# Performance work log

Measured on AMD Instinct MI355X. Metric: run time of the kernel, lower is better.

The kernel has to match this reference:

```python
import jax, jax.numpy as jnp
import numpy as np

B, H, W = 64, 128, 128
PS, G = 8, 16            # patch size, token grid (128//8)
E = 256                  # embed_dim (hidden_dim)
NS, IT, TEMP = 8, 3, 1.0 # num_slots, slot_iters, slot_temperature
V = 10                   # vocab_size
FD = 320                 # full_dim = latent_dim(256) + pose_dim(64)
HEADS, HD = 4, E // 4    # RoPE attn heads / head_dim
N = G * G


def _ln(x, g, b, eps=1e-5):
    m = x.mean(-1, keepdims=True)
    v = ((x - m) ** 2).mean(-1, keepdims=True)
    return (x - m) * jax.lax.rsqrt(v + eps) * g + b


def _conv(x, w, stride):
    return jax.lax.conv_general_dilated(
        x, w, (stride, stride), 'VALID',
        dimension_numbers=('NCHW', 'OIHW', 'NCHW'))


def _rope_tables(g, hd):
    half = hd // 2
    inv = 1.0 / (10000.0 ** (jnp.arange(0, half, 2, dtype=jnp.float32) / half))
    pos = jnp.arange(g, dtype=jnp.float32)
    p = jnp.outer(pos, inv)                                  # [g, half//2]
    e = jnp.concatenate([jnp.sin(p), jnp.cos(p)], axis=-1)   # [g, half]
    ex = jnp.broadcast_to(e[None, :, :], (g, g, half))
    ey = jnp.broadcast_to(e[:, None, :], (g, g, half))
    emb = jnp.concatenate([ey, ex], axis=-1).reshape(g * g, hd)
    return jnp.cos(emb)[None, :, None, :], jnp.sin(emb)[None, :, None, :]


def _apply_rope(x, cos, sin):
    x1, x2 = x[..., 0::2], x[..., 1::2]
    rot = jnp.concatenate([-x2, x1], axis=-1)
    return x * cos + rot * sin


def _gru(x, h, wih, whh, bih, bhh):
    gi = x @ wih.T + bih
    gh = h @ whh.T + bhh
    i_r, i_z, i_n = jnp.split(gi, 3, axis=-1)
    h_r, h_z, h_n = jnp.split(gh, 3, axis=-1)
    r = jax.nn.sigmoid(i_r + h_r)
    z = jax.nn.sigmoid(i_z + h_z)
    n = jnp.tanh(i_n + r * h_n)
    return (1.0 - z) * n + z * h


def setup_inputs() -> dict:
    key = jax.random.key(0)
    ks = iter(jax.random.split(key, 40))

    def nrm(shape, s=0.02):
        return (jax.random.normal(next(ks), shape, jnp.float32) * s)

    state = jax.random.randint(next(ks), (B, 1, H, W), 0, V).astype(jnp.float32)
    return {
        'state': state,
        'conv_w': nrm((E, 12, PS, PS)), 'conv_b': jnp.zeros((E,), jnp.float32),
        'mlp_ln_g': jnp.ones((E,), jnp.float32), 'mlp_ln_b': jnp.zeros((E,), jnp.float32),
        'mlp_w1': nrm((2 * E, E)), 'mlp_b1': jnp.zeros((2 * E,), jnp.float32),
        'mlp_w2': nrm((E, 2 * E)), 'mlp_b2': jnp.zeros((E,), jnp.float32),
        'qkv_w': nrm((3 * E, E)), 'qkv_b': jnp.zeros((3 * E,), jnp.float32),
        'proj_w': nrm((E, E)), 'proj_b': jnp.zeros((E,), jnp.float32),
        'ni_g': jnp.ones((E,), jnp.float32), 'ni_b': jnp.zeros((E,), jnp.float32),
        'ns_g': jnp.ones((FD,), jnp.float32), 'ns_b': jnp.zeros((FD,), jnp.float32),
        'nm_g': jnp.ones((FD,), jnp.float32), 'nm_b': jnp.zeros((FD,), jnp.float32),
        'q_w': nrm((FD, FD)), 'k_w': nrm((FD, E)), 'v_w': nrm((FD, E)),
        'gru_wih': nrm((3 * FD, FD)), 'gru_whh': nrm((3 * FD, FD)),
        'gru_bih': jnp.zeros((3 * FD,), jnp.float32), 'gru_bhh': jnp.zeros((3 * FD,), jnp.float32),
        'smlp_w1': nrm((2 * FD, FD)), 'smlp_b1': jnp.zeros((2 * FD,), jnp.float32),
        'smlp_w2': nrm((FD, 2 * FD)), 'smlp_b2': jnp.zeros((FD,), jnp.float32),
    }


def reference(state, conv_w, conv_b, mlp_ln_g, mlp_ln_b, mlp_w1, mlp_b1,
              mlp_w2, mlp_b2, qkv_w, qkv_b, proj_w, proj_b, ni_g, ni_b,
              ns_g, ns_b, nm_g, nm_b, q_w, k_w, v_w,
              gru_wih, gru_whh, gru_bih, gru_bhh,
              smlp_w1, smlp_b1, smlp_w2, smlp_b2):
    # Sobel edge features on replicate-padded image
    sob_x = jnp.array([[-1., 0., 1.], [-2., 0., 2.], [-1., 0., 1.]], jnp.float32).reshape(1, 1, 3, 3)
    sob_y = jnp.array([[-1., -2., -1.], [0., 0., 0.], [1., 2., 1.]], jnp.float32).reshape(1, 1, 3, 3)
    pad = jnp.pad(state, ((0, 0), (0, 0), (1, 1), (1, 1)), mode='edge')
    sx = _conv(pad, sob_x, 1)
    sy = _conv(pad, sob_y, 1)
    ids = jax.lax.stop_gradient(state)[:, 0].astype(jnp.int32)
    onehot = jax.nn.one_hot(ids, V, dtype=jnp.float32).transpose(0, 3, 1, 2)
    comp = jnp.concatenate([onehot, sx, sy], axis=1)            # [B,12,H,W]

    # Patch embed -> tokens [B,N,E]
    x = _conv(comp, conv_w, PS) + conv_b[None, :, None, None]   # [B,E,G,G]
    x = x.reshape(B, E, N).transpose(0, 2, 1)

    # patch_mlp (LN -> Linear -> GELU -> Linear), no residual
    h = _ln(x, mlp_ln_g, mlp_ln_b)
    h = jax.nn.gelu(h @ mlp_w1.T + mlp_b1, approximate=False)
    x = h @ mlp_w2.T + mlp_b2

    # RoPE self-attention, residual
    cos, sin = _rope_tables(G, HD)
    qkv = (x @ qkv_w.T + qkv_b).reshape(B, N, 3, HEADS, HD)
    q, k, v = qkv[:, :, 0], qkv[:, :, 1], qkv[:, :, 2]          # [B,N,Hh,HD]
    q = _apply_rope(q, cos, sin).transpose(0, 2, 1, 3)          # [B,Hh,N,HD]
    k = _apply_rope(k, cos, sin).transpose(0, 2, 1, 3)
    v = v.transpose(0, 2, 1, 3)
    attn = jax.nn.softmax(jnp.einsum('bhnd,bhmd->bhnm', q, k) * HD ** -0.5, axis=-1)
    ao = jnp.einsum('bhnm,bhmd->bhnd', attn, v).transpose(0, 2, 1, 3).reshape(B, N, E)
    x = x + (ao @ proj_w.T + proj_b)
    x = _ln(x, ni_g, ni_b)

    k_in = x @ k_w.T                                            # [B,N,FD]
    v_in = x @ v_w.T

    # No codebook injected -> zero slot priors
    slots = jnp.zeros((B, NS, FD), jnp.float32)
    sattn = None
    for _ in range(IT):
        slots_prev = slots
        q_s = _ln(slots, ns_g, ns_b) @ q_w.T                    # [B,NS,FD]
        logits = jnp.einsum('bnf,bsf->bns', k_in, q_s) * FD ** -0.5
        sattn = jax.nn.softmax(logits / TEMP, axis=-1)          # over slots
        an = sattn + 1e-8
        an = an / an.sum(axis=1, keepdims=True)                 # normalize over keys
        updates = jnp.einsum('bns,bnf->bsf', an, v_in)          # [B,NS,FD]
        slots = _gru(updates.reshape(-1, FD), slots_prev.reshape(-1, FD),
                     gru_wih, gru_whh, gru_bih, gru_bhh).reshape(B, NS, FD)
        m = _ln(slots, nm_g, nm_b)
        m = jax.nn.gelu(m @ smlp_w1.T + smlp_b1, approximate=False)
        slots = slots + (m @ smlp_w2.T + smlp_b2)

    masks = jax.lax.stop_gradient(sattn).transpose(0, 2, 1).reshape(B, NS, G, G)
    return slots, masks
```

## Files before the change

### kernel.cpp

```cpp
#include <hip/hip_runtime.h>
#include <math.h>

#define BB   64
#define HH   128
#define WW   128
#define GG   16
#define NN   256
#define EE   256
#define FD   320
#define NSL  8
#define NHEAD 4
#define HD   64
#define KIM  768

using short8 = __attribute__((ext_vector_type(8))) short;
using f32x4  = __attribute__((ext_vector_type(4))) float;

__device__ __forceinline__ float sigm(float x) { return 1.0f / (1.0f + expf(-x)); }
__device__ __forceinline__ float gelu_exact(float x) {
    return 0.5f * x * (1.0f + erff(x * 0.70710678118654752f));
}
__device__ __forceinline__ unsigned short f2b(float x) {
    unsigned u = __float_as_uint(x);
    u += 0x7fffu + ((u >> 16) & 1u);
    return (unsigned short)(u >> 16);
}
__device__ __forceinline__ float b2f(unsigned short u) {
    return __uint_as_float(((unsigned)u) << 16);
}
__device__ __forceinline__ void gload_lds16(const void* g, void* lds) {
    __builtin_amdgcn_global_load_lds(
        (const __attribute__((address_space(1))) unsigned int*)g,
        (__attribute__((address_space(3))) unsigned int*)lds, 16, 0, 0);
}
__device__ __forceinline__ void store_el(float* p, float v) { *p = v; }
__device__ __forceinline__ void store_el(unsigned short* p, float v) { *p = f2b(v); }

__global__ __launch_bounds__(256) void cvt_weights(
    const float* __restrict__ w0, const float* __restrict__ w1,
    const float* __restrict__ w2, const float* __restrict__ w3,
    const float* __restrict__ w4, const float* __restrict__ w5,
    const float* __restrict__ w6, const float* __restrict__ w7,
    const float* __restrict__ w8, const float* __restrict__ w9,
    const float* __restrict__ w10, const float* __restrict__ w11,
    unsigned short* __restrict__ dst) {
    int i = blockIdx.x * 256 + threadIdx.x;
    float v;
    if      (i <  196608) v = w0[i];
    else if (i <  327680) v = w1[i - 196608];
    else if (i <  458752) v = w2[i - 327680];
    else if (i <  655360) v = w3[i - 458752];
    else if (i <  720896) v = w4[i - 655360];
    else if (i <  802816) v = w5[i - 720896];
    else if (i <  884736) v = w6[i - 802816];
    else if (i <  987136) v = w7[i - 884736];
    else if (i < 1294336) v = w8[i - 987136];
    else if (i < 1601536) v = w9[i - 1294336];
    else if (i < 1806336) v = w10[i - 1601536];
    else                  v = w11[i - 1806336];
    dst[i] = f2b(v);
}

__global__ __launch_bounds__(256) void cvt_bf16(const float* __restrict__ in,
                                                unsigned short* __restrict__ out, int n) {
    int i = blockIdx.x * 256 + threadIdx.x;
    if (i < n) out[i] = f2b(in[i]);
}

__global__ __launch_bounds__(256) void rope_tab(float* __restrict__ cs,
                                                float* __restrict__ sn) {
    int i = blockIdx.x * 256 + threadIdx.x;
    int d = i & 63, n = i >> 6;
    int pos = (d < 32) ? (n >> 4) : (n & 15);
    int j = d & 31;
    float freq = powf(10000.0f, -(float)(j & 15) / 16.0f);
    float p = (float)pos * freq;
    float ang = (j < 16) ? sinf(p) : cosf(p);
    cs[i] = cosf(ang);
    sn[i] = sinf(ang);
}

__global__ __launch_bounds__(256) void sobel_im2col(const float* __restrict__ state,
                                                    unsigned short* __restrict__ X0) {
    int idx = blockIdx.x * 256 + threadIdx.x;
    if (idx >= BB * HH * WW) return;
    int w = idx % WW;
    int h = (idx / WW) % HH;
    int b = idx / (HH * WW);
    const float* st = state + (long)b * HH * WW;
    auto at = [&](int y, int x) {
        y = min(max(y, 0), HH - 1);
        x = min(max(x, 0), WW - 1);
        return st[y * WW + x];
    };
    float v00 = at(h-1, w-1), v01 = at(h-1, w), v02 = at(h-1, w+1);
    float v10 = at(h,   w-1),                  v12 = at(h,   w+1);
    float v20 = at(h+1, w-1), v21 = at(h+1, w), v22 = at(h+1, w+1);
    float sx = (v02 - v00) + 2.0f * (v12 - v10) + (v22 - v20);
    float sy = (v20 - v00) + 2.0f * (v21 - v01) + (v22 - v02);
    int id = (int)st[h * WW + w];
    int gy = h >> 3, i = h & 7, gx = w >> 3, j = w & 7;
    long row = (long)b * NN + gy * GG + gx;
    unsigned short* xr = X0 + row * KIM + i * 8 + j;
#pragma unroll
    for (int c = 0; c < 10; c++) xr[c * 64] = (id == c) ? 0x3F80u : 0u;
    xr[10 * 64] = f2b(sx);
    xr[11 * 64] = f2b(sy);
}

template <int BM, int BN, int ACT>
__global__ __launch_bounds__(256) void gemm_bf16(
    const unsigned short* __restrict__ A, const unsigned short* __restrict__ W,
    const float* __restrict__ bias, const float* __restrict__ res,
    float* __restrict__ C, unsigned short* __restrict__ Cb,
    int K, long sA, long sW, long sC1, long sC2, int cdiv, int ldc, float scale)
{
    constexpr int WN = BN / 64;
    __shared__ __align__(16) unsigned short As[BM * 32];
    __shared__ __align__(16) unsigned short Bs[BN * 32];
    const int tid = threadIdx.x;
    const int w = tid >> 6, l = tid & 63;
    const int wm = w / WN, wn = w % WN;
    const int bz = blockIdx.z;
    const unsigned short* Ab = A + (long)bz * sA + (long)(blockIdx.y * BM) * K;
    const unsigned short* Wb = W + (long)bz * sW + (long)(blockIdx.x * BN) * K;
    const long offC = (long)(bz / cdiv) * sC1 + (long)(bz % cdiv) * sC2;

    const int rA  = l >> 2;
    const int swz = ((l & 3) ^ ((l >> 3) & 3)) * 8;

    f32x4 acc[4][4] = {};

    for (int k0 = 0; k0 < K; k0 += 32) {
#pragma unroll
        for (int c = 0; c < BM / 64; c++) {
            const int chunk = w * (BM / 64) + c;
            gload_lds16(Ab + (long)(chunk * 16 + rA) * K + k0 + swz, (char*)As + chunk * 1024);
        }
#pragma unroll
        for (int c = 0; c < BN / 64; c++) {
            const int chunk = w * (BN / 64) + c;
            gload_lds16(Wb + (long)(chunk * 16 + rA) * K + k0 + swz, (char*)Bs + chunk * 1024);
        }
        __syncthreads();
        short8 af[4], bfr[4];
#pragma unroll
        for (int m = 0; m < 4; m++) {
            const int row = wm * 64 + m * 16 + (l & 15);
            const int byte = row * 64 + (((l >> 4) ^ ((row >> 1) & 3)) << 4);
            af[m] = *(const short8*)((const char*)As + byte);
        }
#pragma unroll
        for (int n = 0; n < 4; n++) {
            const int row = wn * 64 + n * 16 + (l & 15);
            const int byte = row * 64 + (((l >> 4) ^ ((row >> 1) & 3)) << 4);
            bfr[n] = *(const short8*)((const char*)Bs + byte);
        }
#pragma unroll
        for (int m = 0; m < 4; m++)
#pragma unroll
            for (int n = 0; n < 4; n++)
                acc[m][n] = __builtin_amdgcn_mfma_f32_16x16x32_bf16(af[m], bfr[n], acc[m][n], 0, 0, 0);
        __syncthreads();
    }

    const int crow0 = blockIdx.y * BM + wm * 64;
    const int ccol0 = blockIdx.x * BN + wn * 64;
#pragma unroll
    for (int m = 0; m < 4; m++) {
#pragma unroll
        for (int n = 0; n < 4; n++) {
            const int row = crow0 + m * 16 + ((l >> 4) << 2);
            const int col = ccol0 + n * 16 + (l & 15);
#pragma unroll
            for (int r = 0; r < 4; r++) {
                float v = acc[m][n][r] * scale;
                if (bias) v += bias[col];
                if (ACT == 1) v = gelu_exact(v);
                const long idx = offC + (long)(row + r) * ldc + col;
                if (res) v += res[idx];
                if (C)  C[idx] = v;
                if (Cb) Cb[idx] = f2b(v);
            }
        }
    }
}

template <int ACT>
__global__ __launch_bounds__(256) void gemm_bf16_s(
    const unsigned short* __restrict__ A, const unsigned short* __restrict__ W,
    const float* __restrict__ bias0, const float* __restrict__ bias1,
    const float* __restrict__ res,
    float* __restrict__ C, unsigned short* __restrict__ Cb,
    int K, int N, long sA, long sW, long sC, float scale)
{
    __shared__ __align__(16) unsigned short As[64 * 32];
    __shared__ __align__(16) unsigned short Bs[64 * 32];
    const int tid = threadIdx.x;
    const int w = tid >> 6, l = tid & 63;
    const int gw = l >> 4, l15 = l & 15;
    const int bz = blockIdx.z;
    const unsigned short* Ab = A + (long)bz * sA + (long)(blockIdx.y * 64) * K;
    const unsigned short* Wb = W + (long)bz * sW + (long)(blockIdx.x * 64) * K;
    const float* bias = (bz == 0) ? bias0 : bias1;
    const long offC = (long)bz * sC;

    const int rA  = l >> 2;
    const int swz = ((l & 3) ^ ((l >> 3) & 3)) * 8;

    f32x4 acc[4] = {};

    for (int k0 = 0; k0 < K; k0 += 32) {
        gload_lds16(Ab + (long)(w * 16 + rA) * K + k0 + swz, (char*)As + w * 1024);
        gload_lds16(Wb + (long)(w * 16 + rA) * K + k0 + swz, (char*)Bs + w * 1024);
        __syncthreads();
        short8 af[4];
#pragma unroll
        for (int m = 0; m < 4; m++) {
            const int row = m * 16 + l15;
            af[m] = *(const short8*)((const char*)As + row * 64 + ((gw ^ ((row >> 1) & 3)) << 4));
        }
        const int brow = w * 16 + l15;
        const short8 bf = *(const short8*)((const char*)Bs + brow * 64 + ((gw ^ ((brow >> 1) & 3)) << 4));
#pragma unroll
        for (int m = 0; m < 4; m++)
            acc[m] = __builtin_amdgcn_mfma_f32_16x16x32_bf16(af[m], bf, acc[m], 0, 0, 0);
        __syncthreads();
    }

    const int col = blockIdx.x * 64 + w * 16 + l15;
    const int row0 = blockIdx.y * 64;
#pragma unroll
    for (int m = 0; m < 4; m++) {
        const int row = row0 + m * 16 + (gw << 2);
#pragma unroll
        for (int r = 0; r < 4; r++) {
            float v = acc[m][r] * scale;
            if (bias) v += bias[col];
            if (ACT == 1) v = gelu_exact(v);
            const long idx = offC + (long)(row + r) * N + col;
            if (res) v += res[idx];
            if (C)  C[idx] = v;
            if (Cb) Cb[idx] = f2b(v);
        }
    }
}

template <typename OT>
__global__ __launch_bounds__(256) void ln_rows(const float* __restrict__ X,
                                               OT* __restrict__ Y,
                                               const float* __restrict__ g,
                                               const float* __restrict__ b,
                                               int rows, int D) {
    int gtid = blockIdx.x * 256 + threadIdx.x;
    int row = gtid >> 6;
    int lane = gtid & 63;
    if (row >= rows) return;
    const float* x = X + (long)row * D;
    const int nv = D >> 6;
    float v[5];
    float s = 0.0f;
#pragma unroll 5
    for (int i = 0; i < nv; i++) { v[i] = x[lane + (i << 6)]; s += v[i]; }
#pragma unroll
    for (int o = 32; o; o >>= 1) s += __shfl_down(s, o);
    s = __shfl(s, 0);
    float mean = s / (float)D;
    float s2 = 0.0f;
#pragma unroll 5
    for (int i = 0; i < nv; i++) { float d = v[i] - mean; s2 += d * d; }
#pragma unroll
    for (int o = 32; o; o >>= 1) s2 += __shfl_down(s2, o);
    s2 = __shfl(s2, 0);
    float inv = rsqrtf(s2 / (float)D + 1e-5f);
    OT* y = Y + (long)row * D;
#pragma unroll 5
    for (int i = 0; i < nv; i++) {
        int d = lane + (i << 6);
        store_el(&y[d], (v[i] - mean) * inv * g[d] + b[d]);
    }
}

__global__ __launch_bounds__(256) void gru_ln(const float* __restrict__ GI,
                                              const float* __restrict__ GH,
                                              float* __restrict__ slots,
                                              const float* __restrict__ g,
                                              const float* __restrict__ b,
                                              unsigned short* __restrict__ SLnb) {
    int gtid = blockIdx.x * 256 + threadIdx.x;
    int row = gtid >> 6;
    int lane = gtid & 63;
    const float* gi = GI + (long)row * 960;
    const float* gh = GH + (long)row * 960;
    float* sl = slots + (long)row * FD;
    float h[5];
    float s = 0.0f;
#pragma unroll
    for (int i = 0; i < 5; i++) {
        const int f = lane + (i << 6);
        const float rr = sigm(gi[f] + gh[f]);
        const float z  = sigm(gi[320 + f] + gh[320 + f]);
        const float nn = tanhf(gi[640 + f] + rr * gh[640 + f]);
        const float hn = (1.0f - z) * nn + z * sl[f];
        h[i] = hn;
        s += hn;
        sl[f] = hn;
    }
#pragma unroll
    for (int o = 32; o; o >>= 1) s += __shfl_down(s, o);
    s = __shfl(s, 0);
    const float mean = s * (1.0f / FD);
    float s2 = 0.0f;
#pragma unroll
    for (int i = 0; i < 5; i++) { const float d = h[i] - mean; s2 += d * d; }
#pragma unroll
    for (int o = 32; o; o >>= 1) s2 += __shfl_down(s2, o);
    s2 = __shfl(s2, 0);
    const float inv = rsqrtf(s2 * (1.0f / FD) + 1e-5f);
    unsigned short* y = SLnb + (long)row * FD;
#pragma unroll
    for (int i = 0; i < 5; i++) {
        const int f = lane + (i << 6);
        y[f] = f2b((h[i] - mean) * inv * g[f] + b[f]);
    }
}

__global__ __launch_bounds__(256) void rope_qk(const unsigned short* __restrict__ QKVb,
                                               const float* __restrict__ cs,
                                               const float* __restrict__ sn,
                                               unsigned short* __restrict__ Qr,
                                               unsigned short* __restrict__ Kr) {
    const int rid = blockIdx.x * 256 + threadIdx.x;
    const int n = rid & 255;
    const int h = (rid >> 8) & 3;
    const int b = rid >> 10;
    const unsigned short* src = QKVb + ((long)(b * 256 + n)) * 768 + h * 64;
    float cv[64], sv[64];
#pragma unroll
    for (int i = 0; i < 16; i++) {
        *(float4*)&cv[i * 4] = *(const float4*)(cs + n * 64 + i * 4);
        *(float4*)&sv[i * 4] = *(const float4*)(sn + n * 64 + i * 4);
    }
#pragma unroll
    for (int qk = 0; qk < 2; qk++) {
        const unsigned short* s0 = src + qk * 256;
        unsigned short* dst = (qk == 0 ? Qr : Kr) + (long)rid * 64;
        float x[64];
#pragma unroll
        for (int i = 0; i < 8; i++) {
            short8 v = *(const short8*)(s0 + i * 8);
#pragma unroll
            for (int j = 0; j < 8; j++) x[i * 8 + j] = b2f((unsigned short)v[j]);
        }
        unsigned short o[64];
#pragma unroll
        for (int d = 0; d < 64; d++) {
            const float rot = (d < 32) ? -x[2 * d + 1] : x[2 * (d - 32)];
            o[d] = f2b(x[d] * cv[d] + rot * sv[d]);
        }
#pragma unroll
        for (int i = 0; i < 8; i++)
            *(short8*)(dst + i * 8) = *(short8*)&o[i * 8];
    }
}

__global__ __launch_bounds__(256, 1) void fused_attn(
    const unsigned short* __restrict__ Qr,
    const unsigned short* __restrict__ Kr,
    const unsigned short* __restrict__ QKVb,
    unsigned short* __restrict__ AOb)
{
    __shared__ __align__(16) char SL[49152];
    const int h = blockIdx.x, b = blockIdx.y;
    const int tid = threadIdx.x;
    const int w = tid >> 6, l = tid & 63;
    const int gw = l >> 4, l15 = l & 15;
    const long bh = (long)b * 4 + h;
    const unsigned short* Qb = Qr + bh * NN * 64;
    const unsigned short* Kb = Kr + bh * NN * 64;
// ... 63 lines not shown
        }
        f32x4 acco[4][2] = {};
#pragma unroll
        for (int c = 0; c < 4; c++) {
#pragma unroll
            for (int nfi = 0; nfi < 4; nfi++) {
                const int nf = c * 4 + nfi;
                const int kt = nf >> 1;
                const int gr = (nf & 1) * 2 + (gw >> 1);
                const int lr = l15 + 16 * gr;
                const int j0 = (gw & 1) * 4;
#pragma unroll
                for (int mf = 0; mf < 2; mf++) {
                    uint2 pk;
                    pk.x = (unsigned)f2b(accs[nf][mf][0] * rs[mf]) |
                           ((unsigned)f2b(accs[nf][mf][1] * rs[mf]) << 16);
                    pk.y = (unsigned)f2b(accs[nf][mf][2] * rs[mf]) |
                           ((unsigned)f2b(accs[nf][mf][3] * rs[mf]) << 16);
                    *(uint2*)(Pw + ((kt & 1) * 2 + mf) * 1024 + lr * 16 + j0 * 2) = pk;
                }
            }
#pragma unroll
            for (int kti = 0; kti < 2; kti++) {
                const int kt = c * 2 + kti;
                short8 vf[4];
#pragma unroll
                for (int df = 0; df < 4; df++) {
                    const int d = df * 16 + l15;
                    vf[df] = *(const short8*)(SL + d * 512 + (((kt * 4 + gw) ^ (d & 15)) << 4));
                }
#pragma unroll
                for (int mf = 0; mf < 2; mf++) {
                    const short8 pf = *(const short8*)(Pw + (kti * 2 + mf) * 1024 + l * 16);
#pragma unroll
                    for (int df = 0; df < 4; df++)
                        acco[df][mf] = __builtin_amdgcn_mfma_f32_16x16x32_bf16(vf[df], pf, acco[df][mf], 0, 0, 0);
                }
            }
        }
#pragma unroll
        for (int df = 0; df < 4; df++)
#pragma unroll
            for (int mf = 0; mf < 2; mf++) {
                const int m = mbase + mf * 16 + l15;
                const int d = df * 16 + gw * 4;
                unsigned short o[4];
#pragma unroll
                for (int r = 0; r < 4; r++) o[r] = f2b(acco[df][mf][r]);
                *(uint2*)(AOb + ((long)(b * NN + m) * 256 + h * 64 + d)) = *(uint2*)o;
            }
    }
}

__global__ __launch_bounds__(256) void slot_logits(const float* __restrict__ Kin,
                                                   const float* __restrict__ Qs,
                                                   float* __restrict__ sattn,
                                                   float* __restrict__ sums) {
    const int b = blockIdx.x;
    const int chunk = blockIdx.y;
    __shared__ float qs[NSL][FD];
    __shared__ float colsum[NSL];
    const int tid = threadIdx.x;
    for (int i = tid; i < NSL * FD; i += 256) qs[i / FD][i % FD] = Qs[(long)b * NSL * FD + i];
    if (tid < NSL) colsum[tid] = 0.0f;
    __syncthreads();
    const int wv = tid >> 6, lane = tid & 63;
    float wsum[NSL] = {};
#pragma unroll
    for (int rr = 0; rr < 4; rr++) {
        const int r = chunk * 16 + wv * 4 + rr;
        const float* kr = Kin + ((long)b * NN + r) * FD;
        float acc[NSL] = {};
#pragma unroll
        for (int i = 0; i < 5; i++) {
            const int t = lane + (i << 6);
            const float kv = kr[t];
#pragma unroll
            for (int s = 0; s < NSL; s++) acc[s] = fmaf(kv, qs[s][t], acc[s]);
        }
#pragma unroll
        for (int s = 0; s < NSL; s++)
#pragma unroll
            for (int o = 32; o; o >>= 1) acc[s] += __shfl_down(acc[s], o);
        if (lane == 0) {
            const float scale = 0.055901699437494740f;
            float mx = -1e30f;
#pragma unroll
            for (int s = 0; s < NSL; s++) { acc[s] *= scale; mx = fmaxf(mx, acc[s]); }
            float e[NSL], sum = 0.0f;
#pragma unroll
            for (int s = 0; s < NSL; s++) { e[s] = expf(acc[s] - mx); sum += e[s]; }
            const float rsum = 1.0f / sum;
            float* outp = sattn + ((long)b * NN + r) * NSL;
#pragma unroll
            for (int s = 0; s < NSL; s++) {
                const float pp = e[s] * rsum;
                outp[s] = pp;
                wsum[s] += pp;
            }
        }
    }
    if (lane == 0) {
#pragma unroll
        for (int s = 0; s < NSL; s++) atomicAdd(&colsum[s], wsum[s]);
    }
    __syncthreads();
    if (tid < NSL) atomicAdd(&sums[b * NSL + tid], colsum[tid]);
}

__global__ __launch_bounds__(256) void slot_updates(const float* __restrict__ sattn,
                                                    const float* __restrict__ sums,
                                                    const float* __restrict__ Vin,
                                                    float* __restrict__ Upd) {
    const int b = blockIdx.x;
    const int chunk = blockIdx.y;
    const int t = threadIdx.x;
    __shared__ float an[64][NSL];
    __shared__ float inv_s[NSL];
    if (t < NSL) inv_s[t] = 1.0f / (sums[b * NSL + t] + (float)NN * 1e-8f);
    __syncthreads();
    for (int i = t; i < 64 * NSL; i += 256) {
        const int s = i & 7;
        const int n = i >> 3;
        an[n][s] = (sattn[((long)b * NN + chunk * 64 + n) * NSL + s] + 1e-8f) * inv_s[s];
    }
    __syncthreads();
    float acc[NSL][2] = {};
    const float* vb = Vin + ((long)b * NN + chunk * 64) * FD;
    for (int n = 0; n < 64; n++) {
        const float v1 = vb[(long)n * FD + t];
        const float v2 = (t < 64) ? vb[(long)n * FD + 256 + t] : 0.0f;
#pragma unroll
        for (int s = 0; s < NSL; s++) {
            const float a = an[n][s];
            acc[s][0] = fmaf(a, v1, acc[s][0]);
            acc[s][1] = fmaf(a, v2, acc[s][1]);
        }
    }
    float* ub = Upd + (long)b * NSL * FD;
#pragma unroll
    for (int s = 0; s < NSL; s++) {
        atomicAdd(&ub[s * FD + t], acc[s][0]);
        if (t < 64) atomicAdd(&ub[s * FD + 256 + t], acc[s][1]);
    }
}

__global__ __launch_bounds__(256) void write_out(const float* __restrict__ slots,
                                                 const float* __restrict__ sattn,
                                                 float* __restrict__ out) {
    int idx = blockIdx.x * 256 + threadIdx.x;
    const int SLOT_SZ = BB * NSL * FD;
    const int MASK_SZ = BB * NSL * NN;
    if (idx < SLOT_SZ) {
        out[idx] = slots[idx];
    } else if (idx < SLOT_SZ + MASK_SZ) {
        int i = idx - SLOT_SZ;
        int b = i >> 11;
        int s = (i >> 8) & 7;
        int n = i & 255;
        out[idx] = sattn[((long)b * NN + n) * NSL + s];
    }
}

extern "C" void kernel_launch(void* const* d_in, const int* in_sizes, int n_in,
                              void* d_out, int out_size, void* d_ws, size_t ws_size,
                              hipStream_t stream) {
    const float* state    = (const float*)d_in[0];
    const float* conv_w   = (const float*)d_in[1];
    const float* conv_b   = (const float*)d_in[2];
    const float* mlp_ln_g = (const float*)d_in[3];
    const float* mlp_ln_b = (const float*)d_in[4];
    const float* mlp_w1   = (const float*)d_in[5];
    const float* mlp_b1   = (const float*)d_in[6];
    const float* mlp_w2   = (const float*)d_in[7];
    const float* mlp_b2   = (const float*)d_in[8];
    const float* qkv_w    = (const float*)d_in[9];
    const float* qkv_b    = (const float*)d_in[10];
    const float* proj_w   = (const float*)d_in[11];
    const float* proj_b   = (const float*)d_in[12];
    const float* ni_g     = (const float*)d_in[13];
    const float* ni_b     = (const float*)d_in[14];
    const float* ns_g     = (const float*)d_in[15];
    const float* ns_b     = (const float*)d_in[16];
    const float* nm_g     = (const float*)d_in[17];
    const float* nm_b     = (const float*)d_in[18];
    const float* q_w      = (const float*)d_in[19];
    const float* k_w      = (const float*)d_in[20];
    const float* v_w      = (const float*)d_in[21];
    const float* gru_wih  = (const float*)d_in[22];
    const float* gru_whh  = (const float*)d_in[23];
    const float* gru_bih  = (const float*)d_in[24];
    const float* gru_bhh  = (const float*)d_in[25];
    const float* smlp_w1  = (const float*)d_in[26];
    const float* smlp_b1  = (const float*)d_in[27];
    const float* smlp_w2  = (const float*)d_in[28];
    const float* smlp_b2  = (const float*)d_in[29];

    float* ws = (float*)d_ws;
    const int M = BB * NN;
    typedef unsigned short u16;

    u16*   X0b  = (u16*)(ws + 0L);
    u16*   Qr   = (u16*)(ws + 0L);
    u16*   Kr   = (u16*)(ws + 2097152L);
    float* X1   = ws + 6291456L;
    u16*   XLNb = (u16*)(ws + 10485760L);
    u16*   Hbufb= (u16*)(ws + 12582912L);
    u16*   QKVb = (u16*)(ws + 6291456L);
    u16*   X2b  = (u16*)(ws + 23068672L);
    float* X2   = ws + 31457280L;
    u16*   Xnb  = (u16*)(ws + 31457280L);
    float* X3   = ws + 35651584L;
    float* Slots= ws + 35651584L;
    float* Qs   = ws + 35979264L;
    float* Satt = ws + 36143104L;
    float* Sums = ws + 36274176L;
    float* Upd  = ws + 36274688L;
    float* GI   = ws + 36438528L;
    float* GH   = ws + 36930048L;
    u16*   SLnb = (u16*)(ws + 37421568L);
    u16*   Updb = (u16*)(ws + 37503488L);
    u16*   Slotsb=(u16*)(ws + 37585408L);
    u16*   Mhb  = (u16*)(ws + 37667328L);
    float* Kin  = ws + 39845888L;
    float* Vin  = ws + 45088768L;
    u16*   AOb    = (u16*)(ws + 50331648L);
    u16*   wb     = (u16*)(ws + 52428800L);
    u16*   conv_wb= wb + 0;
    u16*   mlp_w1b= wb + 196608;
    u16*   mlp_w2b= wb + 327680;
    u16*   qkv_wb = wb + 458752;
    u16*   proj_wb= wb + 655360;
    u16*   k_wb   = wb + 720896;
    u16*   v_wb   = wb + 802816;
    u16*   q_wb   = wb + 884736;
    u16*   wihb   = wb + 987136;
    u16*   whhb   = wb + 1294336;
    u16*   smlp1b = wb + 1601536;
    u16*   smlp2b = wb + 1806336;
    float* CS     = ws + 53434368L;
    float* SN     = ws + 53450752L;

    float* out = (float*)d_out;

    auto gemmA = [&](const u16* A, const u16* Wt, const float* bias, const float* res,
                     float* C, u16* Cb, int Mm, int Nn, int Kk, int batch,
                     long sA, long sW, long sC1, long sC2, int cdiv, int ldc,
                     float scale, int act) {
        dim3 grid(Nn / 128, Mm / 128, batch);
        if (act) gemm_bf16<128, 128, 1><<<grid, 256, 0, stream>>>(A, Wt, bias, res, C, Cb, Kk, sA, sW, sC1, sC2, cdiv, ldc, scale);
        else     gemm_bf16<128, 128, 0><<<grid, 256, 0, stream>>>(A, Wt, bias, res, C, Cb, Kk, sA, sW, sC1, sC2, cdiv, ldc, scale);
    };
    auto gemmB = [&](const u16* A, const u16* Wt, float* C, int Mm, int Nn, int Kk) {
        dim3 grid(Nn / 64, Mm / 256, 1);
        gemm_bf16<256, 64, 0><<<grid, 256, 0, stream>>>(A, Wt, nullptr, nullptr, C, nullptr, Kk, 0, 0, 0, 0, 1, Nn, 1.0f);
    };
    auto gemmS = [&](const u16* A, const u16* Wt, const float* b0, const float* b1,
                     const float* res, float* C, u16* Cb, int Mm, int Nn, int Kk,
                     int batch, long sA, long sW, long sC, int act) {
        dim3 grid(Nn / 64, Mm / 64, batch);
        if (act) gemm_bf16_s<1><<<grid, 256, 0, stream>>>(A, Wt, b0, b1, res, C, Cb, Kk, Nn, sA, sW, sC, 1.0f);
        else     gemm_bf16_s<0><<<grid, 256, 0, stream>>>(A, Wt, b0, b1, res, C, Cb, Kk, Nn, sA, sW, sC, 1.0f);
    };

    cvt_weights<<<dim3(2011136 / 256), 256, 0, stream>>>(conv_w, mlp_w1, mlp_w2, qkv_w,
                                                         proj_w, k_w, v_w, q_w,
                                                         gru_wih, gru_whh, smlp_w1, smlp_w2, wb);
    rope_tab<<<dim3(16384 / 256), 256, 0, stream>>>(CS, SN);

    sobel_im2col<<<dim3((BB * HH * WW) / 256), 256, 0, stream>>>(state, X0b);
    gemmA(X0b, conv_wb, conv_b, nullptr, X1, nullptr, M, EE, KIM, 1, 0, 0, 0, 0, 1, EE, 1.0f, 0);
    ln_rows<u16><<<dim3(M * 64 / 256), 256, 0, stream>>>(X1, XLNb, mlp_ln_g, mlp_ln_b, M, EE);
    gemmA(XLNb, mlp_w1b, mlp_b1, nullptr, nullptr, Hbufb, M, 2 * EE, EE, 1, 0, 0, 0, 0, 1, 2 * EE, 1.0f, 1);
    gemmA(Hbufb, mlp_w2b, mlp_b2, nullptr, X2, X2b, M, EE, 2 * EE, 1, 0, 0, 0, 0, 1, EE, 1.0f, 0);
    gemmA(X2b, qkv_wb, qkv_b, nullptr, nullptr, QKVb, M, 3 * EE, EE, 1, 0, 0, 0, 0, 1, 3 * EE, 1.0f, 0);
    rope_qk<<<dim3(65536 / 256), 256, 0, stream>>>(QKVb, CS, SN, Qr, Kr);
    fused_attn<<<dim3(NHEAD, BB), 256, 0, stream>>>(Qr, Kr, QKVb, AOb);
    gemmA(AOb, proj_wb, proj_b, X2, X3, nullptr, M, EE, EE, 1, 0, 0, 0, 0, 1, EE, 1.0f, 0);
    ln_rows<u16><<<dim3(M * 64 / 256), 256, 0, stream>>>(X3, Xnb, ni_g, ni_b, M, EE);
    gemmB(Xnb, k_wb, Kin, M, FD, EE);
    gemmB(Xnb, v_wb, Vin, M, FD, EE);
    hipMemsetAsync(Slots, 0, (size_t)BB * NSL * FD * sizeof(float), stream);
    hipMemsetAsync(Slotsb, 0, (size_t)BB * NSL * FD * sizeof(u16), stream);
    for (int it = 0; it < 3; it++) {
        ln_rows<u16><<<dim3(512 * 64 / 256), 256, 0, stream>>>(Slots, SLnb, ns_g, ns_b, 512, FD);
        gemmS(SLnb, q_wb, nullptr, nullptr, nullptr, Qs, nullptr, 512, FD, FD, 1, 0, 0, 0, 0);
        hipMemsetAsync(Sums, 0, (size_t)BB * NSL * sizeof(float), stream);
        slot_logits<<<dim3(BB, 16), 256, 0, stream>>>(Kin, Qs, Satt, Sums);
        hipMemsetAsync(Upd, 0, (size_t)BB * NSL * FD * sizeof(float), stream);
        slot_updates<<<dim3(BB, 4), 256, 0, stream>>>(Satt, Sums, Vin, Upd);
        cvt_bf16<<<dim3(163840 / 256), 256, 0, stream>>>(Upd, Updb, 163840);
        gemmS(Updb, wihb, gru_bih, gru_bhh, nullptr, GI, nullptr, 512, 960, FD,
              2, 163840, 307200, 491520, 0);
        gru_ln<<<dim3(512 * 64 / 256), 256, 0, stream>>>(GI, GH, Slots, nm_g, nm_b, SLnb);
        gemmS(SLnb, smlp1b, smlp_b1, nullptr, nullptr, nullptr, Mhb, 512, 2 * FD, FD, 1, 0, 0, 0, 1);
        gemmS(Mhb, smlp2b, smlp_b2, nullptr, Slots, Slots, Slotsb, 512, FD, 2 * FD, 1, 0, 0, 0, 0);
    }
    write_out<<<dim3((BB * NSL * FD + BB * NSL * NN + 255) / 256), 256, 0, stream>>>(Slots, Satt, out);
}
```

Before: 644.1 us.

## Fuse slot-attention iterations into one per-batch persistent kernel with MFMA

Replaces the per-iteration chain of small launches (LN, q GEMM, logits, updates, convert, GRU GEMMs, GRU/LN, MLP GEMMs, output copy) with a single kernel, one block per batch element. The block keeps slots in LDS across all three iterations and does every small GEMM with bf16 MFMA. K and V projections are now written as bf16, with V transposed, so the fused kernel can stream them directly. This removes many launches, memsets and global round-trips. The cost is only 64 blocks of work, each reading weights straight from global memory, so per-block latency and low occupancy may dominate.

```diff
diff --git a/kernel.cpp b/kernel.cpp
--- a/kernel.cpp
+++ b/kernel.cpp
@@ -12,6 +12,10 @@
 #define NHEAD 4
 #define HD   64
 #define KIM  768
+
+#define K320P 328
+#define K256P 264
+#define K640P 648
 
 using short8 = __attribute__((ext_vector_type(8))) short;
 using f32x4  = __attribute__((ext_vector_type(4))) float;
@@ -61,12 +65,6 @@
     dst[i] = f2b(v);
 }
 
-__global__ __launch_bounds__(256) void cvt_bf16(const float* __restrict__ in,
-                                                unsigned short* __restrict__ out, int n) {
-    int i = blockIdx.x * 256 + threadIdx.x;
-    if (i < n) out[i] = f2b(in[i]);
-}
-
 __global__ __launch_bounds__(256) void rope_tab(float* __restrict__ cs,
                                                 float* __restrict__ sn) {
     int i = blockIdx.x * 256 + threadIdx.x;
@@ -113,7 +111,8 @@
     const unsigned short* __restrict__ A, const unsigned short* __restrict__ W,
     const float* __restrict__ bias, const float* __restrict__ res,
     float* __restrict__ C, unsigned short* __restrict__ Cb,
-    int K, long sA, long sW, long sC1, long sC2, int cdiv, int ldc, float scale)
+    int K, long sA, long sW, long sC1, long sC2, int cdiv, int ldc, float scale,
+    int tr)
 {
     constexpr int WN = BN / 64;
     __shared__ __align__(16) unsigned short As[BM * 32];
@@ -180,68 +179,12 @@
                 const long idx = offC + (long)(row + r) * ldc + col;
                 if (res) v += res[idx];
                 if (C)  C[idx] = v;
-                if (Cb) Cb[idx] = f2b(v);
-            }
-        }
-    }
-}
-
-template <int ACT>
-__global__ __launch_bounds__(256) void gemm_bf16_s(
-    const unsigned short* __restrict__ A, const unsigned short* __restrict__ W,
-    const float* __restrict__ bias0, const float* __restrict__ bias1,
-    const float* __restrict__ res,
-    float* __restrict__ C, unsigned short* __restrict__ Cb,
-    int K, int N, long sA, long sW, long sC, float scale)
-{
-    __shared__ __align__(16) unsigned short As[64 * 32];
-    __shared__ __align__(16) unsigned short Bs[64 * 32];
-    const int tid = threadIdx.x;
-    const int w = tid >> 6, l = tid & 63;
-    const int gw = l >> 4, l15 = l & 15;
-    const int bz = blockIdx.z;
-    const unsigned short* Ab = A + (long)bz * sA + (long)(blockIdx.y * 64) * K;
-    const unsigned short* Wb = W + (long)bz * sW + (long)(blockIdx.x * 64) * K;
-    const float* bias = (bz == 0) ? bias0 : bias1;
-    const long offC = (long)bz * sC;
-
-    const int rA  = l >> 2;
-    const int swz = ((l & 3) ^ ((l >> 3) & 3)) * 8;
-
-    f32x4 acc[4] = {};
-
-    for (int k0 = 0; k0 < K; k0 += 32) {
-        gload_lds16(Ab + (long)(w * 16 + rA) * K + k0 + swz, (char*)As + w * 1024);
-        gload_lds16(Wb + (long)(w * 16 + rA) * K + k0 + swz, (char*)Bs + w * 1024);
-        __syncthreads();
-        short8 af[4];
-#pragma unroll
-        for (int m = 0; m < 4; m++) {
-            const int row = m * 16 + l15;
-            af[m] = *(const short8*)((const char*)As + row * 64 + ((gw ^ ((row >> 1) & 3)) << 4));
-        }
-        const int brow = w * 16 + l15;
-        const short8 bf = *(const short8*)((const char*)Bs + brow * 64 + ((gw ^ ((brow >> 1) & 3)) << 4));
-#pragma unroll
-        for (int m = 0; m < 4; m++)
-            acc[m] = __builtin_amdgcn_mfma_f32_16x16x32_bf16(af[m], bf, acc[m], 0, 0, 0);
-        __syncthreads();
-    }
-
-    const int col = blockIdx.x * 64 + w * 16 + l15;
-    const int row0 = blockIdx.y * 64;
-#pragma unroll
-    for (int m = 0; m < 4; m++) {
-        const int row = row0 + m * 16 + (gw << 2);
-#pragma unroll
-        for (int r = 0; r < 4; r++) {
-            float v = acc[m][r] * scale;
-            if (bias) v += bias[col];
-            if (ACT == 1) v = gelu_exact(v);
-            const long idx = offC + (long)(row + r) * N + col;
-            if (res) v += res[idx];
-            if (C)  C[idx] = v;
-            if (Cb) Cb[idx] = f2b(v);
+                if (Cb) {
+                    long cidx = tr ? (((long)((row + r) >> 8) * ldc + col) * 256 + ((row + r) & 255))
+                                   : idx;
+                    Cb[cidx] = f2b(v);
+                }
+            }
         }
     }
 }
@@ -281,50 +224,6 @@
     }
 }
 
-__global__ __launch_bounds__(256) void gru_ln(const float* __restrict__ GI,
-                                              const float* __restrict__ GH,
-                                              float* __restrict__ slots,
-                                              const float* __restrict__ g,
-                                              const float* __restrict__ b,
-                                              unsigned short* __restrict__ SLnb) {
-    int gtid = blockIdx.x * 256 + threadIdx.x;
-    int row = gtid >> 6;
-    int lane = gtid & 63;
-    const float* gi = GI + (long)row * 960;
-    const float* gh = GH + (long)row * 960;
-    float* sl = slots + (long)row * FD;
-    float h[5];
-    float s = 0.0f;
-#pragma unroll
-    for (int i = 0; i < 5; i++) {
-        const int f = lane + (i << 6);
-        const float rr = sigm(gi[f] + gh[f]);
-        const float z  = sigm(gi[320 + f] + gh[320 + f]);
-        const float nn = tanhf(gi[640 + f] + rr * gh[640 + f]);
-        const float hn = (1.0f - z) * nn + z * sl[f];
-        h[i] = hn;
-        s += hn;
-        sl[f] = hn;
-    }
-#pragma unroll
-    for (int o = 32; o; o >>= 1) s += __shfl_down(s, o);
-    s = __shfl(s, 0);
-    const float mean = s * (1.0f / FD);
-    float s2 = 0.0f;
-#pragma unroll
-    for (int i = 0; i < 5; i++) { const float d = h[i] - mean; s2 += d * d; }
-#pragma unroll
-    for (int o = 32; o; o >>= 1) s2 += __shfl_down(s2, o);
-    s2 = __shfl(s2, 0);
-    const float inv = rsqrtf(s2 * (1.0f / FD) + 1e-5f);
-    unsigned short* y = SLnb + (long)row * FD;
-#pragma unroll
-    for (int i = 0; i < 5; i++) {
-        const int f = lane + (i << 6);
-        y[f] = f2b((h[i] - mean) * inv * g[f] + b[f]);
-    }
-}
-
 __global__ __launch_bounds__(256) void rope_qk(const unsigned short* __restrict__ QKVb,
                                                const float* __restrict__ cs,
                                                const float* __restrict__ sn,
@@ -494,114 +393,279 @@
     }
 }
 
-__global__ __launch_bounds__(256) void slot_logits(const float* __restrict__ Kin,
-                                                   const float* __restrict__ Qs,
-                                                   float* __restrict__ sattn,
-                                                   float* __restrict__ sums) {
+__global__ __launch_bounds__(256, 1) void fused_slots(
+    const unsigned short* __restrict__ Kinb,
+    const unsigned short* __restrict__ Vtb,
+    const unsigned short* __restrict__ q_wb,
+    const unsigned short* __restrict__ wihb,
+    const unsigned short* __restrict__ whhb,
+    const unsigned short* __restrict__ s1b,
+    const unsigned short* __restrict__ s2b,
+    const float* __restrict__ ns_g, const float* __restrict__ ns_b,
+    const float* __restrict__ nm_g, const float* __restrict__ nm_b,
+    const float* __restrict__ bih, const float* __restrict__ bhh,
+    const float* __restrict__ sb1, const float* __restrict__ sb2,
+    float* __restrict__ out)
+{
+    __shared__ float slots[8][320];
+    __shared__ __align__(16) unsigned short slotsb[16][K320P];
+    __shared__ __align__(16) unsigned short sln[16][K320P];
+    __shared__ __align__(16) char D[27136];
+    __shared__ float colsum[8];
+    __shared__ float wred[4][8];
+
+    unsigned short* q_s  = (unsigned short*)D;
+    unsigned short* updm = (unsigned short*)D;
+    float*          P    = (float*)(D + 10496);
+    unsigned short* anT  = (unsigned short*)(D + 18688);
+    unsigned short* Mh   = (unsigned short*)D;
+
     const int b = blockIdx.x;
-    const int chunk = blockIdx.y;
-    __shared__ float qs[NSL][FD];
-    __shared__ float colsum[NSL];
     const int tid = threadIdx.x;
-    for (int i = tid; i < NSL * FD; i += 256) qs[i / FD][i % FD] = Qs[(long)b * NSL * FD + i];
-    if (tid < NSL) colsum[tid] = 0.0f;
+    const int w = tid >> 6, l = tid & 63;
+    const int gw = l >> 4, l15 = l & 15;
+
+    for (int i = tid; i < 8 * 320; i += 256) ((float*)slots)[i] = 0.0f;
+    for (int i = tid; i < 8 * K320P; i += 256) {
+        ((unsigned short*)slotsb)[8 * K320P + i] = 0;
+        ((unsigned short*)sln)[8 * K320P + i] = 0;
+    }
+    for (int i = tid; i < 8 * K256P; i += 256) anT[8 * K256P + i] = 0;
     __syncthreads();
-    const int wv = tid >> 6, lane = tid & 63;
-    float wsum[NSL] = {};
-#pragma unroll
-    for (int rr = 0; rr < 4; rr++) {
-        const int r = chunk * 16 + wv * 4 + rr;
-        const float* kr = Kin + ((long)b * NN + r) * FD;
-        float acc[NSL] = {};
-#pragma unroll
-        for (int i = 0; i < 5; i++) {
-            const int t = lane + (i << 6);
-            const float kv = kr[t];
-#pragma unroll
-            for (int s = 0; s < NSL; s++) acc[s] = fmaf(kv, qs[s][t], acc[s]);
-        }
-#pragma unroll
-        for (int s = 0; s < NSL; s++)
-#pragma unroll
-            for (int o = 32; o; o >>= 1) acc[s] += __shfl_down(acc[s], o);
-        if (lane == 0) {
-            const float scale = 0.055901699437494740f;
-            float mx = -1e30f;
-#pragma unroll
-            for (int s = 0; s < NSL; s++) { acc[s] *= scale; mx = fmaxf(mx, acc[s]); }
-            float e[NSL], sum = 0.0f;
-#pragma unroll
-            for (int s = 0; s < NSL; s++) { e[s] = expf(acc[s] - mx); sum += e[s]; }
-            const float rsum = 1.0f / sum;
-            float* outp = sattn + ((long)b * NN + r) * NSL;
-#pragma unroll
-            for (int s = 0; s < NSL; s++) {
-                const float pp = e[s] * rsum;
-                outp[s] = pp;
-                wsum[s] += pp;
-            }
-        }
-    }
-    if (lane == 0) {
-#pragma unroll
-        for (int s = 0; s < NSL; s++) atomicAdd(&colsum[s], wsum[s]);
-    }
-    __syncthreads();
-    if (tid < NSL) atomicAdd(&sums[b * NSL + tid], colsum[tid]);
-}
-
-__global__ __launch_bounds__(256) void slot_updates(const float* __restrict__ sattn,
-                                                    const float* __restrict__ sums,
-                                                    const float* __restrict__ Vin,
-                                                    float* __restrict__ Upd) {
-    const int b = blockIdx.x;
-    const int chunk = blockIdx.y;
-    const int t = threadIdx.x;
-    __shared__ float an[64][NSL];
-    __shared__ float inv_s[NSL];
-    if (t < NSL) inv_s[t] = 1.0f / (sums[b * NSL + t] + (float)NN * 1e-8f);
-    __syncthreads();
-    for (int i = t; i < 64 * NSL; i += 256) {
-        const int s = i & 7;
-        const int n = i >> 3;
-        an[n][s] = (sattn[((long)b * NN + chunk * 64 + n) * NSL + s] + 1e-8f) * inv_s[s];
-    }
-    __syncthreads();
-    float acc[NSL][2] = {};
-    const float* vb = Vin + ((long)b * NN + chunk * 64) * FD;
-    for (int n = 0; n < 64; n++) {
-        const float v1 = vb[(long)n * FD + t];
-        const float v2 = (t < 64) ? vb[(long)n * FD + 256 + t] : 0.0f;
-#pragma unroll
-        for (int s = 0; s < NSL; s++) {
-            const float a = an[n][s];
-            acc[s][0] = fmaf(a, v1, acc[s][0]);
-            acc[s][1] = fmaf(a, v2, acc[s][1]);
-        }
-    }
-    float* ub = Upd + (long)b * NSL * FD;
-#pragma unroll
-    for (int s = 0; s < NSL; s++) {
-        atomicAdd(&ub[s * FD + t], acc[s][0]);
-        if (t < 64) atomicAdd(&ub[s * FD + 256 + t], acc[s][1]);
-    }
-}
-
-__global__ __launch_bounds__(256) void write_out(const float* __restrict__ slots,
-                                                 const float* __restrict__ sattn,
-                                                 float* __restrict__ out) {
-    int idx = blockIdx.x * 256 + threadIdx.x;
-    const int SLOT_SZ = BB * NSL * FD;
-    const int MASK_SZ = BB * NSL * NN;
-    if (idx < SLOT_SZ) {
-        out[idx] = slots[idx];
-    } else if (idx < SLOT_SZ + MASK_SZ) {
-        int i = idx - SLOT_SZ;
-        int b = i >> 11;
-        int s = (i >> 8) & 7;
-        int n = i & 255;
-        out[idx] = sattn[((long)b * NN + n) * NSL + s];
-    }
+
+    for (int it = 0; it < 3; ++it) {
+        for (int rr = w; rr < 8; rr += 4) {
+            const float* x = slots[rr];
+            float v[5]; float s = 0.0f;
+#pragma unroll
+            for (int i = 0; i < 5; i++) { v[i] = x[l + (i << 6)]; s += v[i]; }
+#pragma unroll
+            for (int o = 32; o; o >>= 1) s += __shfl_down(s, o);
+            s = __shfl(s, 0);
+            const float mean = s * (1.0f / FD);
+            float s2 = 0.0f;
+#pragma unroll
+            for (int i = 0; i < 5; i++) { const float d = v[i] - mean; s2 += d * d; }
+#pragma unroll
+            for (int o = 32; o; o >>= 1) s2 += __shfl_down(s2, o);
+            s2 = __shfl(s2, 0);
+            const float inv = rsqrtf(s2 * (1.0f / FD) + 1e-5f);
+#pragma unroll
+            for (int i = 0; i < 5; i++) {
+                const int f = l + (i << 6);
+                sln[rr][f] = f2b((v[i] - mean) * inv * ns_g[f] + ns_b[f]);
+                slotsb[rr][f] = f2b(v[i]);
+            }
+        }
+        __syncthreads();
+
+        {
+            f32x4 acc[5] = {};
+            for (int k0 = 0; k0 < 320; k0 += 32) {
+                const short8 af = *(const short8*)&sln[l15][k0 + gw * 8];
+#pragma unroll
+                for (int j = 0; j < 5; j++) {
+                    const int n0 = (w * 5 + j) * 16;
+                    const short8 bf = *(const short8*)(q_wb + (long)(n0 + l15) * 320 + k0 + gw * 8);
+                    acc[j] = __builtin_amdgcn_mfma_f32_16x16x32_bf16(af, bf, acc[j], 0, 0, 0);
+                }
+            }
+#pragma unroll
+            for (int j = 0; j < 5; j++) {
+                const int col = (w * 5 + j) * 16 + l15;
+#pragma unroll
+                for (int r = 0; r < 4; r++)
+                    q_s[(gw * 4 + r) * K320P + col] = f2b(acc[j][r]);
+            }
+        }
+        __syncthreads();
+
+        {
+            f32x4 acc[4] = {};
+            const unsigned short* Kb = Kinb + (long)b * 256 * 320;
+            for (int k0 = 0; k0 < 320; k0 += 32) {
+                const short8 bf = *(const short8*)&q_s[l15 * K320P + k0 + gw * 8];
+#pragma unroll
+                for (int mt = 0; mt < 4; mt++) {
+                    const int row = (w * 4 + mt) * 16 + l15;
+                    const short8 af = *(const short8*)(Kb + (long)row * 320 + k0 + gw * 8);
+                    acc[mt] = __builtin_amdgcn_mfma_f32_16x16x32_bf16(af, bf, acc[mt], 0, 0, 0);
+                }
+            }
+            float psum = 0.0f;
+#pragma unroll
+            for (int mt = 0; mt < 4; mt++) {
+#pragma unroll
+                for (int r = 0; r < 4; r++) {
+                    const float val = acc[mt][r] * 0.055901699437494740f;
+                    float mx = val;
+                    mx = fmaxf(mx, __shfl_xor(mx, 1));
+                    mx = fmaxf(mx, __shfl_xor(mx, 2));
+                    mx = fmaxf(mx, __shfl_xor(mx, 4));
+                    const float e = expf(val - mx);
+                    float sum = e;
+                    sum += __shfl_xor(sum, 1);
+                    sum += __shfl_xor(sum, 2);
+                    sum += __shfl_xor(sum, 4);
+                    const float p = e / sum;
+                    const int t = (w * 4 + mt) * 16 + gw * 4 + r;
+                    if (l15 < 8) P[t * 8 + l15] = p;
+                    psum += p;
+                }
+            }
+            psum += __shfl_down(psum, 32);
+            psum += __shfl_down(psum, 16);
+            if (gw == 0 && l15 < 8) wred[w][l15] = psum;
+        }
+        __syncthreads();
+        if (tid < 8) colsum[tid] = wred[0][tid] + wred[1][tid] + wred[2][tid] + wred[3][tid]
+                                   + (float)NN * 1e-8f;
+        __syncthreads();
+
+        if (it == 2) {
+            const int n = tid;
+#pragma unroll
+            for (int s = 0; s < 8; s++)
+                out[163840 + b * 2048 + s * 256 + n] = P[n * 8 + s];
+        }
+
+        {
+            const int n = tid;
+#pragma unroll
+            for (int s = 0; s < 8; s++)
+                anT[s * K256P + n] = f2b((P[n * 8 + s] + 1e-8f) / colsum[s]);
+        }
+        __syncthreads();
+
+        {
+            f32x4 acc[5] = {};
+            const unsigned short* Vb = Vtb + (long)b * 320 * 256;
+            for (int k0 = 0; k0 < 256; k0 += 32) {
+                const short8 af = *(const short8*)&anT[l15 * K256P + k0 + gw * 8];
+#pragma unroll
+                for (int j = 0; j < 5; j++) {
+                    const int f0 = (w * 5 + j) * 16;
+                    const short8 bf = *(const short8*)(Vb + (long)(f0 + l15) * 256 + k0 + gw * 8);
+                    acc[j] = __builtin_amdgcn_mfma_f32_16x16x32_bf16(af, bf, acc[j], 0, 0, 0);
+                }
+            }
+#pragma unroll
+            for (int j = 0; j < 5; j++) {
+                const int col = (w * 5 + j) * 16 + l15;
+#pragma unroll
+                for (int r = 0; r < 4; r++)
+                    updm[(gw * 4 + r) * K320P + col] = f2b(acc[j][r]);
+            }
+        }
+        __syncthreads();
+
+        {
+            f32x4 gi[3][5] = {}, gh[3][5] = {};
+            for (int k0 = 0; k0 < 320; k0 += 32) {
+                const short8 ai = *(const short8*)&updm[l15 * K320P + k0 + gw * 8];
+                const short8 ah = *(const short8*)&slotsb[l15][k0 + gw * 8];
+#pragma unroll
+                for (int g = 0; g < 3; g++)
+#pragma unroll
+                    for (int j = 0; j < 5; j++) {
+                        const int n0 = (g * 20 + w * 5 + j) * 16;
+                        const short8 bi = *(const short8*)(wihb + (long)(n0 + l15) * 320 + k0 + gw * 8);
+                        gi[g][j] = __builtin_amdgcn_mfma_f32_16x16x32_bf16(ai, bi, gi[g][j], 0, 0, 0);
+                        const short8 bh2 = *(const short8*)(whhb + (long)(n0 + l15) * 320 + k0 + gw * 8);
+                        gh[g][j] = __builtin_amdgcn_mfma_f32_16x16x32_bf16(ah, bh2, gh[g][j], 0, 0, 0);
+                    }
+            }
+#pragma unroll
+            for (int j = 0; j < 5; j++) {
+                const int f = (w * 5 + j) * 16 + l15;
+#pragma unroll
+                for (int r = 0; r < 4; r++) {
+                    const int s = gw * 4 + r;
+                    if (s < 8) {
+                        const float gir = gi[0][j][r] + bih[f],       ghr = gh[0][j][r] + bhh[f];
+                        const float giz = gi[1][j][r] + bih[320 + f], ghz = gh[1][j][r] + bhh[320 + f];
+                        const float gin = gi[2][j][r] + bih[640 + f], ghn = gh[2][j][r] + bhh[640 + f];
+                        const float rr2 = sigm(gir + ghr);
+                        const float z   = sigm(giz + ghz);
+                        const float nn2 = tanhf(gin + rr2 * ghn);
+                        slots[s][f] = (1.0f - z) * nn2 + z * slots[s][f];
+                    }
+                }
+            }
+        }
+        __syncthreads();
+
+        for (int rr = w; rr < 8; rr += 4) {
+            const float* x = slots[rr];
+            float v[5]; float s = 0.0f;
+#pragma unroll
+            for (int i = 0; i < 5; i++) { v[i] = x[l + (i << 6)]; s += v[i]; }
+#pragma unroll
+            for (int o = 32; o; o >>= 1) s += __shfl_down(s, o);
+            s = __shfl(s, 0);
+            const float mean = s * (1.0f / FD);
+            float s2 = 0.0f;
+#pragma unroll
+            for (int i = 0; i < 5; i++) { const float d = v[i] - mean; s2 += d * d; }
+#pragma unroll
+            for (int o = 32; o; o >>= 1) s2 += __shfl_down(s2, o);
+            s2 = __shfl(s2, 0);
+            const float inv = rsqrtf(s2 * (1.0f / FD) + 1e-5f);
+#pragma unroll
+            for (int i = 0; i < 5; i++) {
+                const int f = l + (i << 6);
+                sln[rr][f] = f2b((v[i] - mean) * inv * nm_g[f] + nm_b[f]);
+            }
+        }
+        __syncthreads();
+
+        {
+            f32x4 acc[10] = {};
+            for (int k0 = 0; k0 < 320; k0 += 32) {
+                const short8 af = *(const short8*)&sln[l15][k0 + gw * 8];
+#pragma unroll
+                for (int j = 0; j < 10; j++) {
+                    const int n0 = (w * 10 + j) * 16;
+                    const short8 bf = *(const short8*)(s1b + (long)(n0 + l15) * 320 + k0 + gw * 8);
+                    acc[j] = __builtin_amdgcn_mfma_f32_16x16x32_bf16(af, bf, acc[j], 0, 0, 0);
+                }
+            }
+#pragma unroll
+            for (int j = 0; j < 10; j++) {
+                const int col = (w * 10 + j) * 16 + l15;
+#pragma unroll
+                for (int r = 0; r < 4; r++)
+                    Mh[(gw * 4 + r) * K640P + col] = f2b(gelu_exact(acc[j][r] + sb1[col]));
+            }
+        }
+        __syncthreads();
+
+        {
+            f32x4 acc[5] = {};
+            for (int k0 = 0; k0 < 640; k0 += 32) {
+                const short8 af = *(const short8*)&Mh[l15 * K640P + k0 + gw * 8];
+#pragma unroll
+                for (int j = 0; j < 5; j++) {
+                    const int n0 = (w * 5 + j) * 16;
+                    const short8 bf = *(const short8*)(s2b + (long)(n0 + l15) * 640 + k0 + gw * 8);
+                    acc[j] = __builtin_amdgcn_mfma_f32_16x16x32_bf16(af, bf, acc[j], 0, 0, 0);
+                }
+            }
+#pragma unroll
+            for (int j = 0; j < 5; j++) {
+                const int col = (w * 5 + j) * 16 + l15;
+#pragma unroll
+                for (int r = 0; r < 4; r++) {
+                    const int s = gw * 4 + r;
+                    if (s < 8) slots[s][col] += acc[j][r] + sb2[col];
+                }
+            }
+        }
+        __syncthreads();
+    }
+
+    for (int i = tid; i < 2560; i += 256)
+        out[b * 2560 + i] = ((const float*)slots)[i];
 }
 
 extern "C" void kernel_launch(void* const* d_in, const int* in_sizes, int n_in,
@@ -653,19 +717,8 @@
     float* X2   = ws + 31457280L;
     u16*   Xnb  = (u16*)(ws + 31457280L);
     float* X3   = ws + 35651584L;
-    float* Slots= ws + 35651584L;
-    float* Qs   = ws + 35979264L;
-    float* Satt = ws + 36143104L;
-    float* Sums = ws + 36274176L;
-    float* Upd  = ws + 36274688L;
-    float* GI   = ws + 36438528L;
-    float* GH   = ws + 36930048L;
-    u16*   SLnb = (u16*)(ws + 37421568L);
-    u16*   Updb = (u16*)(ws + 37503488L);
-    u16*   Slotsb=(u16*)(ws + 37585408L);
-    u16*   Mhb  = (u16*)(ws + 37667328L);
-    float* Kin  = ws + 39845888L;
-    float* Vin  = ws + 45088768L;
+    u16*   Kinb = (u16*)(ws + 39845888L);
+    u16*   Vtb  = (u16*)(ws + 42467328L);
     u16*   AOb    = (u16*)(ws + 50331648L);
     u16*   wb     = (u16*)(ws + 52428800L);
     u16*   conv_wb= wb + 0;
@@ -690,19 +743,12 @@
                      long sA, long sW, long sC1, long sC2, int cdiv, int ldc,
                      float scale, int act) {
         dim3 grid(Nn / 128, Mm / 128, batch);
-        if (act) gemm_bf16<128, 128, 1><<<grid, 256, 0, stream>>>(A, Wt, bias, res, C, Cb, Kk, sA, sW, sC1, sC2, cdiv, ldc, scale);
-        else     gemm_bf16<128, 128, 0><<<grid, 256, 0, stream>>>(A, Wt, bias, res, C, Cb, Kk, sA, sW, sC1, sC2, cdiv, ldc, scale);
+        if (act) gemm_bf16<128, 128, 1><<<grid, 256, 0, stream>>>(A, Wt, bias, res, C, Cb, Kk, sA, sW, sC1, sC2, cdiv, ldc, scale, 0);
+        else     gemm_bf16<128, 128, 0><<<grid, 256, 0, stream>>>(A, Wt, bias, res, C, Cb, Kk, sA, sW, sC1, sC2, cdiv, ldc, scale, 0);
     };
-    auto gemmB = [&](const u16* A, const u16* Wt, float* C, int Mm, int Nn, int Kk) {
+    auto gemmB = [&](const u16* A, const u16* Wt, u16* Cb, int Mm, int Nn, int Kk, int tr) {
         dim3 grid(Nn / 64, Mm / 256, 1);
-        gemm_bf16<256, 64, 0><<<grid, 256, 0, stream>>>(A, Wt, nullptr, nullptr, C, nullptr, Kk, 0, 0, 0, 0, 1, Nn, 1.0f);
-    };
-    auto gemmS = [&](const u16* A, const u16* Wt, const float* b0, const float* b1,
-                     const float* res, float* C, u16* Cb, int Mm, int Nn, int Kk,
-                     int batch, long sA, long sW, long sC, int act) {
-        dim3 grid(Nn / 64, Mm / 64, batch);
-        if (act) gemm_bf16_s<1><<<grid, 256, 0, stream>>>(A, Wt, b0, b1, res, C, Cb, Kk, Nn, sA, sW, sC, 1.0f);
-        else     gemm_bf16_s<0><<<grid, 256, 0, stream>>>(A, Wt, b0, b1, res, C, Cb, Kk, Nn, sA, sW, sC, 1.0f);
+        gemm_bf16<256, 64, 0><<<grid, 256, 0, stream>>>(A, Wt, nullptr, nullptr, nullptr, Cb, Kk, 0, 0, 0, 0, 1, Nn, 1.0f, tr);
     };
 
     cvt_weights<<<dim3(2011136 / 256), 256, 0, stream>>>(conv_w, mlp_w1, mlp_w2, qkv_w,
@@ -720,23 +766,9 @@
     fused_attn<<<dim3(NHEAD, BB), 256, 0, stream>>>(Qr, Kr, QKVb, AOb);
     gemmA(AOb, proj_wb, proj_b, X2, X3, nullptr, M, EE, EE, 1, 0, 0, 0, 0, 1, EE, 1.0f, 0);
     ln_rows<u16><<<dim3(M * 64 / 256), 256, 0, stream>>>(X3, Xnb, ni_g, ni_b, M, EE);
-    gemmB(Xnb, k_wb, Kin, M, FD, EE);
-    gemmB(Xnb, v_wb, Vin, M, FD, EE);
-    hipMemsetAsync(Slots, 0, (size_t)BB * NSL * FD * sizeof(float), stream);
-    hipMemsetAsync(Slotsb, 0, (size_t)BB * NSL * FD * sizeof(u16), stream);
-    for (int it = 0; it < 3; it++) {
-        ln_rows<u16><<<dim3(512 * 64 / 256), 256, 0, stream>>>(Slots, SLnb, ns_g, ns_b, 512, FD);
-        gemmS(SLnb, q_wb, nullptr, nullptr, nullptr, Qs, nullptr, 512, FD, FD, 1, 0, 0, 0, 0);
-        hipMemsetAsync(Sums, 0, (size_t)BB * NSL * sizeof(float), stream);
-        slot_logits<<<dim3(BB, 16), 256, 0, stream>>>(Kin, Qs, Satt, Sums);
-        hipMemsetAsync(Upd, 0, (size_t)BB * NSL * FD * sizeof(float), stream);
-        slot_updates<<<dim3(BB, 4), 256, 0, stream>>>(Satt, Sums, Vin, Upd);
-        cvt_bf16<<<dim3(163840 / 256), 256, 0, stream>>>(Upd, Updb, 163840);
-        gemmS(Updb, wihb, gru_bih, gru_bhh, nullptr, GI, nullptr, 512, 960, FD,
-              2, 163840, 307200, 491520, 0);
-        gru_ln<<<dim3(512 * 64 / 256), 256, 0, stream>>>(GI, GH, Slots, nm_g, nm_b, SLnb);
-        gemmS(SLnb, smlp1b, smlp_b1, nullptr, nullptr, nullptr, Mhb, 512, 2 * FD, FD, 1, 0, 0, 0, 1);
-        gemmS(Mhb, smlp2b, smlp_b2, nullptr, Slots, Slots, Slotsb, 512, FD, 2 * FD, 1, 0, 0, 0, 0);
-    }
-    write_out<<<dim3((BB * NSL * FD + BB * NSL * NN + 255) / 256), 256, 0, stream>>>(Slots, Satt, out);
-}
+    gemmB(Xnb, k_wb, Kinb, M, FD, EE, 0);
+    gemmB(Xnb, v_wb, Vtb, M, FD, EE, 1);
+    fused_slots<<<dim3(BB), 256, 0, stream>>>(Kinb, Vtb, q_wb, wihb, whhb, smlp1b, smlp2b,
+                                              ns_g, ns_b, nm_g, nm_b,
+                                              gru_bih, gru_bhh, smlp_b1, smlp_b2, out);
+}
```

New measurement: 1.169 ms. 81.5% more time.
